# Kernel optimization log

Measured on AMD Instinct MI355X. Metric: run time of the kernel, lower is better.

The kernel has to match this reference:

```python
import jax, jax.numpy as jnp
import numpy as np

B, N, F, E = 2, 50000, 128, 500000


def setup_inputs() -> dict:
    key = jax.random.key(0)
    ks = jax.random.split(key, 7)
    x0 = jax.random.normal(ks[0], (B, N, F), dtype=jnp.float32)
    dst = jax.random.randint(ks[1], (E,), 0, N, dtype=jnp.int32)
    src = jax.random.randint(ks[2], (E,), 0, N, dtype=jnp.int32)
    # torch Linear weights: [out_features, in_features]
    w0 = jax.random.normal(ks[3], (F, 2 * F), dtype=jnp.float32) * 0.05
    b0 = jax.random.normal(ks[4], (F,), dtype=jnp.float32) * 0.05
    w1 = jax.random.normal(ks[5], (F, F), dtype=jnp.float32) * 0.05
    b1 = jax.random.normal(ks[6], (F,), dtype=jnp.float32) * 0.05
    return {"x0": x0, "dst": dst, "src": src, "w0": w0, "b0": b0, "w1": w1, "b1": b1}


def reference(x0, dst, src, w0, b0, w1, b1):
    n = x0.shape[1]
    # gather source node features per edge: [B, E, F] -> [E, B, F] for segment ops
    xe = jnp.transpose(x0[:, src], (1, 0, 2))
    # scatter-reduce over destination nodes (include_self=False semantics)
    s = jax.ops.segment_sum(xe, dst, num_segments=n)                      # [N, B, F]
    mx = jax.ops.segment_max(xe, dst, num_segments=n)                     # [N, B, F]
    cnt = jax.ops.segment_sum(jnp.ones((dst.shape[0],), x0.dtype), dst, num_segments=n)  # [N]
    has_edge = (cnt > 0)[:, None, None]
    x0t = jnp.transpose(x0, (1, 0, 2))                                    # [N, B, F]
    # nodes with no incoming edges keep their original values
    mean = jnp.where(has_edge, s / jnp.maximum(cnt, 1.0)[:, None, None], x0t)
    amax = jnp.where(has_edge, mx, x0t)
    x = jnp.concatenate([mean, amax], axis=-1)                            # [N, B, 2F]
    h = jax.nn.relu(jnp.einsum('nbf,of->nbo', x, w0) + b0)
    # dropout is identity in eval mode
    out = x0t + jnp.einsum('nbf,of->nbo', h, w1) + b1
    return jnp.transpose(out, (1, 0, 2))                                  # [B, N, F]
```

## Files before the change

kernel.cpp:

```cpp
#include <hip/hip_runtime.h>

#define NN 50000
#define FF 128
constexpr int NBF2 = NN * 256;
constexpr int CAP  = 64;

typedef __attribute__((ext_vector_type(4))) short short4v;
typedef __attribute__((ext_vector_type(8))) short short8;
typedef __attribute__((ext_vector_type(4))) float floatx4;

__device__ __forceinline__ unsigned short f2bf(float x) {
    unsigned int u = __float_as_uint(x);
    unsigned int r = (u + 0x7fff + ((u >> 16) & 1)) >> 16;
    return (unsigned short)r;
}
__device__ __forceinline__ float bf2f(short x) {
    return __uint_as_float(((unsigned int)(unsigned short)x) << 16);
}

__global__ __launch_bounds__(256)
void convert_fill(const int* __restrict__ dst, const int* __restrict__ src, int E,
                  const float* __restrict__ x0,
                  const float* __restrict__ w0, const float* __restrict__ w1,
                  int* __restrict__ cursor, int* __restrict__ esrc,
                  unsigned short* __restrict__ x0b,
                  unsigned short* __restrict__ w0b, unsigned short* __restrict__ w1b) {
    int i = blockIdx.x * 256 + threadIdx.x;
    if (i < E) {
        int d = dst[i];
        int pos = atomicAdd(&cursor[d], 1);
        if (pos < CAP) esrc[d * CAP + pos] = src[i];
    }
    int stride = gridDim.x * 256;
    for (int p = i; p < NBF2 / 4; p += stride) {
        int v0 = p * 4;
        int n = v0 >> 8;
        int b = (v0 >> 7) & 1;
        int f = v0 & 127;
        const float4 in = *(const float4*)&x0[(b * NN + n) * FF + f];
        short4v o = { (short)f2bf(in.x), (short)f2bf(in.y), (short)f2bf(in.z), (short)f2bf(in.w) };
        *(short4v*)&x0b[v0] = o;
    }
    if (i < 128 * 256) w0b[i] = f2bf(w0[i]);
    if (i < 128 * 128) w1b[i] = f2bf(w1[i]);
}

constexpr int NPB = 16;
constexpr int XCP = 256 + 8;
constexpr int HSP = 128 + 8;

__global__ __launch_bounds__(256, 4)
void fused_gcn(const unsigned short* __restrict__ x0b,
               const float* __restrict__ x0,
               const int* __restrict__ deg,
               const int* __restrict__ esrc,
               const unsigned short* __restrict__ w0b,
               const float* __restrict__ b0,
               const unsigned short* __restrict__ w1b,
               const float* __restrict__ b1,
               float* __restrict__ out) {
    __shared__ unsigned short xc[32 * XCP];
    __shared__ int sl_hs[32 * HSP / 2];
    __shared__ int cum[17];
    int* sl = sl_hs;
    unsigned short* hs = (unsigned short*)sl_hs;

    int t = threadIdx.x;
    int q = t >> 6;
    int l = t & 63;
    int n0 = blockIdx.x * NPB;

    if (t < 16) cum[t + 1] = min(deg[n0 + t], CAP);
    if (t == 16) cum[0] = 0;
    __syncthreads();
    if (t == 0) {
        int run = 0;
        for (int i = 1; i <= 16; ++i) { run += cum[i]; cum[i] = run; }
    }
    __syncthreads();

    int T = cum[16];
    for (int i = t; i < T + 8; i += 256) {
        if (i < T) {
            int j = 0;
            while (cum[j + 1] <= i) ++j;
            sl[i] = (j << 16) | esrc[(n0 + j) * CAP + (i - cum[j])];
        } else {
            sl[i] = (16 << 16) | 0xFFFF;
        }
    }
    __syncthreads();

    int l4 = l * 4;
    int bb = l >> 5;
    int ff = (l & 31) * 4;
    const float NEG_INF = __int_as_float(0xFF800000);

    int jb = q * 4;
    int nb = n0 + jb;
    int eS = __builtin_amdgcn_readfirstlane(cum[jb]);
    int eE = __builtin_amdgcn_readfirstlane(cum[jb + 4]);

    float sA0=0,sA1=0,sA2=0,sA3=0, sB0=0,sB1=0,sB2=0,sB3=0;
    float sC0=0,sC1=0,sC2=0,sC3=0, sD0=0,sD1=0,sD2=0,sD3=0;
    float mA0=NEG_INF,mA1=NEG_INF,mA2=NEG_INF,mA3=NEG_INF;
    float mB0=NEG_INF,mB1=NEG_INF,mB2=NEG_INF,mB3=NEG_INF;
    float mC0=NEG_INF,mC1=NEG_INF,mC2=NEG_INF,mC3=NEG_INF;
    float mD0=NEG_INF,mD1=NEG_INF,mD2=NEG_INF,mD3=NEG_INF;

#define GATH_K(k) \
    int u##k = __builtin_amdgcn_readfirstlane(sl[e + k]); \
    short4v r##k = *(const short4v*)&x0b[(unsigned)(u##k & 0xffff) * 256 + l4];

#define ACC_K(k) { \
    int ja = u##k >> 16; \
    if ((ja >> 2) == q) { \
        float v0=bf2f(r##k[0]), v1=bf2f(r##k[1]), v2=bf2f(r##k[2]), v3=bf2f(r##k[3]); \
        int g = ja & 3; \
        if (g == 0)      { sA0+=v0;sA1+=v1;sA2+=v2;sA3+=v3; mA0=fmaxf(mA0,v0);mA1=fmaxf(mA1,v1);mA2=fmaxf(mA2,v2);mA3=fmaxf(mA3,v3); } \
        else if (g == 1) { sB0+=v0;sB1+=v1;sB2+=v2;sB3+=v3; mB0=fmaxf(mB0,v0);mB1=fmaxf(mB1,v1);mB2=fmaxf(mB2,v2);mB3=fmaxf(mB3,v3); } \
        else if (g == 2) { sC0+=v0;sC1+=v1;sC2+=v2;sC3+=v3; mC0=fmaxf(mC0,v0);mC1=fmaxf(mC1,v1);mC2=fmaxf(mC2,v2);mC3=fmaxf(mC3,v3); } \
        else             { sD0+=v0;sD1+=v1;sD2+=v2;sD3+=v3; mD0=fmaxf(mD0,v0);mD1=fmaxf(mD1,v1);mD2=fmaxf(mD2,v2);mD3=fmaxf(mD3,v3); } \
    } }

    for (int e = eS; e < eE; e += 8) {
        GATH_K(0) GATH_K(1) GATH_K(2) GATH_K(3)
        GATH_K(4) GATH_K(5) GATH_K(6) GATH_K(7)
        ACC_K(0) ACC_K(1) ACC_K(2) ACC_K(3)
        ACC_K(4) ACC_K(5) ACC_K(6) ACC_K(7)
    }
#undef GATH_K
#undef ACC_K

#define FINAL_G(g, S0,S1,S2,S3, M0,M1,M2,M3) { \
    int dgx = __builtin_amdgcn_readfirstlane(cum[jb + g + 1] - cum[jb + g]); \
    float me0,me1,me2,me3,a0,a1,a2,a3; \
    if (dgx > 0) { \
        float inv = 1.0f / (float)dgx; \
        me0=S0*inv; me1=S1*inv; me2=S2*inv; me3=S3*inv; \
        a0=M0; a1=M1; a2=M2; a3=M3; \
    } else { \
        short4v rr = *(const short4v*)&x0b[(nb + g) * 256 + l4]; \
        me0=a0=bf2f(rr[0]); me1=a1=bf2f(rr[1]); me2=a2=bf2f(rr[2]); me3=a3=bf2f(rr[3]); \
    } \
    int row = (jb + g) * 2 + bb; \
    short4v mv = { (short)f2bf(me0),(short)f2bf(me1),(short)f2bf(me2),(short)f2bf(me3) }; \
    short4v av = { (short)f2bf(a0),(short)f2bf(a1),(short)f2bf(a2),(short)f2bf(a3) }; \
    *(short4v*)&xc[row * XCP + ff]       = mv; \
    *(short4v*)&xc[row * XCP + 128 + ff] = av; \
}
    FINAL_G(0, sA0,sA1,sA2,sA3, mA0,mA1,mA2,mA3)
    FINAL_G(1, sB0,sB1,sB2,sB3, mB0,mB1,mB2,mB3)
    FINAL_G(2, sC0,sC1,sC2,sC3, mC0,mC1,mC2,mC3)
    FINAL_G(3, sD0,sD1,sD2,sD3, mD0,mD1,mD2,mD3)
#undef FINAL_G
    __syncthreads();

    int m    = l & 15;
    int quad = l >> 4;
    int rowbase = (q >> 1) * 16;
    int colbase = (q & 1) * 64;

    floatx4 acc[4];
#pragma unroll
    for (int ct = 0; ct < 4; ++ct) acc[ct] = (floatx4){0.f, 0.f, 0.f, 0.f};
#pragma unroll
    for (int ks = 0; ks < 8; ++ks) {
        short8 a = *(const short8*)&xc[(rowbase + m) * XCP + ks * 32 + quad * 8];
#pragma unroll
        for (int ct = 0; ct < 4; ++ct) {
            short8 bf = *(const short8*)&w0b[(colbase + ct * 16 + m) * 256 + ks * 32 + quad * 8];
            acc[ct] = __builtin_amdgcn_mfma_f32_16x16x32_bf16(a, bf, acc[ct], 0, 0, 0);
        }
    }
#pragma unroll
    for (int ct = 0; ct < 4; ++ct) {
        int col = colbase + ct * 16 + m;
        float bias = b0[col];
#pragma unroll
        for (int r = 0; r < 4; ++r) {
            int row = rowbase + quad * 4 + r;
            hs[row * HSP + col] = f2bf(fmaxf(acc[ct][r] + bias, 0.0f));
        }
    }
    __syncthreads();

    floatx4 acc2[4];
#pragma unroll
    for (int ct = 0; ct < 4; ++ct) acc2[ct] = (floatx4){0.f, 0.f, 0.f, 0.f};
#pragma unroll
    for (int ks = 0; ks < 4; ++ks) {
        short8 a = *(const short8*)&hs[(rowbase + m) * HSP + ks * 32 + quad * 8];
#pragma unroll
        for (int ct = 0; ct < 4; ++ct) {
            short8 bf = *(const short8*)&w1b[(colbase + ct * 16 + m) * 128 + ks * 32 + quad * 8];
            acc2[ct] = __builtin_amdgcn_mfma_f32_16x16x32_bf16(a, bf, acc2[ct], 0, 0, 0);
        }
    }
#pragma unroll
    for (int ct = 0; ct < 4; ++ct) {
        int col = colbase + ct * 16 + m;
        float bias = b1[col];
#pragma unroll
        for (int r = 0; r < 4; ++r) {
            int row = rowbase + quad * 4 + r;
            int n  = n0 + (row >> 1);
            int b2 = row & 1;
            int oi = (b2 * NN + n) * FF + col;
            out[oi] = x0[oi] + bias + acc2[ct][r];
        }
    }
}

extern "C" void kernel_launch(void* const* d_in, const int* in_sizes, int n_in,
                              void* d_out, int out_size, void* d_ws, size_t ws_size,
                              hipStream_t stream) {
    const float* x0  = (const float*)d_in[0];
    const int*   dst = (const int*)d_in[1];
    const int*   src = (const int*)d_in[2];
    const float* w0  = (const float*)d_in[3];
    const float* b0  = (const float*)d_in[4];
    const float* w1  = (const float*)d_in[5];
    const float* b1  = (const float*)d_in[6];
    float* out = (float*)d_out;
    int E = in_sizes[1];

    int* cursor = (int*)d_ws;
    int* esrc   = cursor + NN;
    unsigned short* x0b = (unsigned short*)(esrc + (size_t)NN * CAP);
    unsigned short* w0b = x0b + NBF2;
    unsigned short* w1b = w0b + 128 * 256;

    int eb = (E + 255) / 256;

    hipMemsetAsync(cursor, 0, (size_t)NN * sizeof(int), stream);
    convert_fill<<<eb, 256, 0, stream>>>(dst, src, E, x0, w0, w1, cursor, esrc, x0b, w0b, w1b);
    fused_gcn<<<NN / NPB, 256, 0, stream>>>(x0b, x0, cursor, esrc, w0b, b0, w1b, b1, out);
}
```

Before: 245.7 us.

## Gather fp32 features directly and halve nodes per block

Drops the bf16 copy of x0 that the preprocessing kernel built, so the fused kernel now gathers fp32 rows straight from x0 in its native [B,N,F] layout. This removes a full read-and-write pass over x0, but each gathered element now costs twice the bytes. Nodes per block fall from 16 to 8, which shrinks the MFMA tile to one 16-row tile per block, cuts LDS use and accumulator registers, and raises the occupancy hint to 7. Each block now loads the weight matrices for half as many rows, so weight reloads per node double.

```diff
diff --git a/kernel.cpp b/kernel.cpp
--- a/kernel.cpp
+++ b/kernel.cpp
@@ -2,8 +2,7 @@
 
 #define NN 50000
 #define FF 128
-constexpr int NBF2 = NN * 256;
-constexpr int CAP  = 64;
+constexpr int CAP = 64;
 
 typedef __attribute__((ext_vector_type(4))) short short4v;
 typedef __attribute__((ext_vector_type(8))) short short8;
@@ -14,44 +13,28 @@
     unsigned int r = (u + 0x7fff + ((u >> 16) & 1)) >> 16;
     return (unsigned short)r;
 }
-__device__ __forceinline__ float bf2f(short x) {
-    return __uint_as_float(((unsigned int)(unsigned short)x) << 16);
-}
 
 __global__ __launch_bounds__(256)
-void convert_fill(const int* __restrict__ dst, const int* __restrict__ src, int E,
-                  const float* __restrict__ x0,
-                  const float* __restrict__ w0, const float* __restrict__ w1,
-                  int* __restrict__ cursor, int* __restrict__ esrc,
-                  unsigned short* __restrict__ x0b,
-                  unsigned short* __restrict__ w0b, unsigned short* __restrict__ w1b) {
+void edge_fill(const int* __restrict__ dst, const int* __restrict__ src, int E,
+               const float* __restrict__ w0, const float* __restrict__ w1,
+               int* __restrict__ cursor, int* __restrict__ esrc,
+               unsigned short* __restrict__ w0b, unsigned short* __restrict__ w1b) {
     int i = blockIdx.x * 256 + threadIdx.x;
     if (i < E) {
         int d = dst[i];
         int pos = atomicAdd(&cursor[d], 1);
         if (pos < CAP) esrc[d * CAP + pos] = src[i];
     }
-    int stride = gridDim.x * 256;
-    for (int p = i; p < NBF2 / 4; p += stride) {
-        int v0 = p * 4;
-        int n = v0 >> 8;
-        int b = (v0 >> 7) & 1;
-        int f = v0 & 127;
-        const float4 in = *(const float4*)&x0[(b * NN + n) * FF + f];
-        short4v o = { (short)f2bf(in.x), (short)f2bf(in.y), (short)f2bf(in.z), (short)f2bf(in.w) };
-        *(short4v*)&x0b[v0] = o;
-    }
     if (i < 128 * 256) w0b[i] = f2bf(w0[i]);
     if (i < 128 * 128) w1b[i] = f2bf(w1[i]);
 }
 
-constexpr int NPB = 16;
+constexpr int NPB = 8;
 constexpr int XCP = 256 + 8;
 constexpr int HSP = 128 + 8;
 
-__global__ __launch_bounds__(256, 4)
-void fused_gcn(const unsigned short* __restrict__ x0b,
-               const float* __restrict__ x0,
+__global__ __launch_bounds__(256, 7)
+void fused_gcn(const float* __restrict__ x0,
                const int* __restrict__ deg,
                const int* __restrict__ esrc,
                const unsigned short* __restrict__ w0b,
@@ -59,9 +42,9 @@
                const unsigned short* __restrict__ w1b,
                const float* __restrict__ b1,
                float* __restrict__ out) {
-    __shared__ unsigned short xc[32 * XCP];
-    __shared__ int sl_hs[32 * HSP / 2];
-    __shared__ int cum[17];
+    __shared__ unsigned short xc[16 * XCP];
+    __shared__ int sl_hs[16 * HSP / 2];
+    __shared__ int cum[9];
     int* sl = sl_hs;
     unsigned short* hs = (unsigned short*)sl_hs;
 
@@ -70,57 +53,55 @@
     int l = t & 63;
     int n0 = blockIdx.x * NPB;
 
-    if (t < 16) cum[t + 1] = min(deg[n0 + t], CAP);
-    if (t == 16) cum[0] = 0;
+    if (t < 8) cum[t + 1] = min(deg[n0 + t], CAP);
+    if (t == 8) cum[0] = 0;
     __syncthreads();
     if (t == 0) {
         int run = 0;
-        for (int i = 1; i <= 16; ++i) { run += cum[i]; cum[i] = run; }
-    }
-    __syncthreads();
-
-    int T = cum[16];
+        for (int i = 1; i <= 8; ++i) { run += cum[i]; cum[i] = run; }
+    }
+    __syncthreads();
+
+    int T = cum[8];
     for (int i = t; i < T + 8; i += 256) {
         if (i < T) {
             int j = 0;
             while (cum[j + 1] <= i) ++j;
             sl[i] = (j << 16) | esrc[(n0 + j) * CAP + (i - cum[j])];
         } else {
-            sl[i] = (16 << 16) | 0xFFFF;
-        }
-    }
-    __syncthreads();
-
-    int l4 = l * 4;
+            sl[i] = (NPB << 16);
+        }
+    }
+    __syncthreads();
+
     int bb = l >> 5;
     int ff = (l & 31) * 4;
+    const float* xrow = x0 + (bb * NN) * FF + ff;
     const float NEG_INF = __int_as_float(0xFF800000);
 
-    int jb = q * 4;
+    int jb = q * 2;
     int nb = n0 + jb;
     int eS = __builtin_amdgcn_readfirstlane(cum[jb]);
-    int eE = __builtin_amdgcn_readfirstlane(cum[jb + 4]);
+    int eE = __builtin_amdgcn_readfirstlane(cum[jb + 2]);
 
     float sA0=0,sA1=0,sA2=0,sA3=0, sB0=0,sB1=0,sB2=0,sB3=0;
-    float sC0=0,sC1=0,sC2=0,sC3=0, sD0=0,sD1=0,sD2=0,sD3=0;
     float mA0=NEG_INF,mA1=NEG_INF,mA2=NEG_INF,mA3=NEG_INF;
     float mB0=NEG_INF,mB1=NEG_INF,mB2=NEG_INF,mB3=NEG_INF;
-    float mC0=NEG_INF,mC1=NEG_INF,mC2=NEG_INF,mC3=NEG_INF;
-    float mD0=NEG_INF,mD1=NEG_INF,mD2=NEG_INF,mD3=NEG_INF;
 
 #define GATH_K(k) \
     int u##k = __builtin_amdgcn_readfirstlane(sl[e + k]); \
-    short4v r##k = *(const short4v*)&x0b[(unsigned)(u##k & 0xffff) * 256 + l4];
+    float4 r##k = *(const float4*)&xrow[(u##k & 0xffff) << 7];
 
 #define ACC_K(k) { \
     int ja = u##k >> 16; \
-    if ((ja >> 2) == q) { \
-        float v0=bf2f(r##k[0]), v1=bf2f(r##k[1]), v2=bf2f(r##k[2]), v3=bf2f(r##k[3]); \
-        int g = ja & 3; \
-        if (g == 0)      { sA0+=v0;sA1+=v1;sA2+=v2;sA3+=v3; mA0=fmaxf(mA0,v0);mA1=fmaxf(mA1,v1);mA2=fmaxf(mA2,v2);mA3=fmaxf(mA3,v3); } \
-        else if (g == 1) { sB0+=v0;sB1+=v1;sB2+=v2;sB3+=v3; mB0=fmaxf(mB0,v0);mB1=fmaxf(mB1,v1);mB2=fmaxf(mB2,v2);mB3=fmaxf(mB3,v3); } \
-        else if (g == 2) { sC0+=v0;sC1+=v1;sC2+=v2;sC3+=v3; mC0=fmaxf(mC0,v0);mC1=fmaxf(mC1,v1);mC2=fmaxf(mC2,v2);mC3=fmaxf(mC3,v3); } \
-        else             { sD0+=v0;sD1+=v1;sD2+=v2;sD3+=v3; mD0=fmaxf(mD0,v0);mD1=fmaxf(mD1,v1);mD2=fmaxf(mD2,v2);mD3=fmaxf(mD3,v3); } \
+    if ((ja >> 1) == q) { \
+        if ((ja & 1) == 0) { \
+            sA0+=r##k.x; sA1+=r##k.y; sA2+=r##k.z; sA3+=r##k.w; \
+            mA0=fmaxf(mA0,r##k.x); mA1=fmaxf(mA1,r##k.y); mA2=fmaxf(mA2,r##k.z); mA3=fmaxf(mA3,r##k.w); \
+        } else { \
+            sB0+=r##k.x; sB1+=r##k.y; sB2+=r##k.z; sB3+=r##k.w; \
+            mB0=fmaxf(mB0,r##k.x); mB1=fmaxf(mB1,r##k.y); mB2=fmaxf(mB2,r##k.z); mB3=fmaxf(mB3,r##k.w); \
+        } \
     } }
 
     for (int e = eS; e < eE; e += 8) {
@@ -140,8 +121,8 @@
         me0=S0*inv; me1=S1*inv; me2=S2*inv; me3=S3*inv; \
         a0=M0; a1=M1; a2=M2; a3=M3; \
     } else { \
-        short4v rr = *(const short4v*)&x0b[(nb + g) * 256 + l4]; \
-        me0=a0=bf2f(rr[0]); me1=a1=bf2f(rr[1]); me2=a2=bf2f(rr[2]); me3=a3=bf2f(rr[3]); \
+        float4 rr = *(const float4*)&xrow[(nb + g) << 7]; \
+        me0=a0=rr.x; me1=a1=rr.y; me2=a2=rr.z; me3=a3=rr.w; \
     } \
     int row = (jb + g) * 2 + bb; \
     short4v mv = { (short)f2bf(me0),(short)f2bf(me1),(short)f2bf(me2),(short)f2bf(me3) }; \
@@ -151,59 +132,56 @@
 }
     FINAL_G(0, sA0,sA1,sA2,sA3, mA0,mA1,mA2,mA3)
     FINAL_G(1, sB0,sB1,sB2,sB3, mB0,mB1,mB2,mB3)
-    FINAL_G(2, sC0,sC1,sC2,sC3, mC0,mC1,mC2,mC3)
-    FINAL_G(3, sD0,sD1,sD2,sD3, mD0,mD1,mD2,mD3)
 #undef FINAL_G
     __syncthreads();
 
     int m    = l & 15;
     int quad = l >> 4;
-    int rowbase = (q >> 1) * 16;
-    int colbase = (q & 1) * 64;
-
-    floatx4 acc[4];
-#pragma unroll
-    for (int ct = 0; ct < 4; ++ct) acc[ct] = (floatx4){0.f, 0.f, 0.f, 0.f};
+    int colbase = q * 32;
+
+    floatx4 acc[2];
+#pragma unroll
+    for (int ct = 0; ct < 2; ++ct) acc[ct] = (floatx4){0.f, 0.f, 0.f, 0.f};
 #pragma unroll
     for (int ks = 0; ks < 8; ++ks) {
-        short8 a = *(const short8*)&xc[(rowbase + m) * XCP + ks * 32 + quad * 8];
-#pragma unroll
-        for (int ct = 0; ct < 4; ++ct) {
-            short8 bf = *(const short8*)&w0b[(colbase + ct * 16 + m) * 256 + ks * 32 + quad * 8];
-            acc[ct] = __builtin_amdgcn_mfma_f32_16x16x32_bf16(a, bf, acc[ct], 0, 0, 0);
-        }
-    }
-#pragma unroll
-    for (int ct = 0; ct < 4; ++ct) {
+        short8 a = *(const short8*)&xc[m * XCP + ks * 32 + quad * 8];
+#pragma unroll
+        for (int ct = 0; ct < 2; ++ct) {
+            short8 bfr = *(const short8*)&w0b[(colbase + ct * 16 + m) * 256 + ks * 32 + quad * 8];
+            acc[ct] = __builtin_amdgcn_mfma_f32_16x16x32_bf16(a, bfr, acc[ct], 0, 0, 0);
+        }
+    }
+#pragma unroll
+    for (int ct = 0; ct < 2; ++ct) {
         int col = colbase + ct * 16 + m;
         float bias = b0[col];
 #pragma unroll
         for (int r = 0; r < 4; ++r) {
-            int row = rowbase + quad * 4 + r;
+            int row = quad * 4 + r;
             hs[row * HSP + col] = f2bf(fmaxf(acc[ct][r] + bias, 0.0f));
         }
     }
     __syncthreads();
 
-    floatx4 acc2[4];
-#pragma unroll
-    for (int ct = 0; ct < 4; ++ct) acc2[ct] = (floatx4){0.f, 0.f, 0.f, 0.f};
+    floatx4 acc2[2];
+#pragma unroll
+    for (int ct = 0; ct < 2; ++ct) acc2[ct] = (floatx4){0.f, 0.f, 0.f, 0.f};
 #pragma unroll
     for (int ks = 0; ks < 4; ++ks) {
-        short8 a = *(const short8*)&hs[(rowbase + m) * HSP + ks * 32 + quad * 8];
-#pragma unroll
-        for (int ct = 0; ct < 4; ++ct) {
-            short8 bf = *(const short8*)&w1b[(colbase + ct * 16 + m) * 128 + ks * 32 + quad * 8];
-            acc2[ct] = __builtin_amdgcn_mfma_f32_16x16x32_bf16(a, bf, acc2[ct], 0, 0, 0);
-        }
-    }
-#pragma unroll
-    for (int ct = 0; ct < 4; ++ct) {
+        short8 a = *(const short8*)&hs[m * HSP + ks * 32 + quad * 8];
+#pragma unroll
+        for (int ct = 0; ct < 2; ++ct) {
+            short8 bfr = *(const short8*)&w1b[(colbase + ct * 16 + m) * 128 + ks * 32 + quad * 8];
+            acc2[ct] = __builtin_amdgcn_mfma_f32_16x16x32_bf16(a, bfr, acc2[ct], 0, 0, 0);
+        }
+    }
+#pragma unroll
+    for (int ct = 0; ct < 2; ++ct) {
         int col = colbase + ct * 16 + m;
         float bias = b1[col];
 #pragma unroll
         for (int r = 0; r < 4; ++r) {
-            int row = rowbase + quad * 4 + r;
+            int row = quad * 4 + r;
             int n  = n0 + (row >> 1);
             int b2 = row & 1;
             int oi = (b2 * NN + n) * FF + col;
@@ -227,13 +205,12 @@
 
     int* cursor = (int*)d_ws;
     int* esrc   = cursor + NN;
-    unsigned short* x0b = (unsigned short*)(esrc + (size_t)NN * CAP);
-    unsigned short* w0b = x0b + NBF2;
+    unsigned short* w0b = (unsigned short*)(esrc + (size_t)NN * CAP);
     unsigned short* w1b = w0b + 128 * 256;
 
     int eb = (E + 255) / 256;
 
     hipMemsetAsync(cursor, 0, (size_t)NN * sizeof(int), stream);
-    convert_fill<<<eb, 256, 0, stream>>>(dst, src, E, x0, w0, w1, cursor, esrc, x0b, w0b, w1b);
-    fused_gcn<<<NN / NPB, 256, 0, stream>>>(x0b, x0, cursor, esrc, w0b, b0, w1b, b1, out);
-}
+    edge_fill<<<eb, 256, 0, stream>>>(dst, src, E, w0, w1, cursor, esrc, w0b, w1b);
+    fused_gcn<<<NN / NPB, 256, 0, stream>>>(x0, cursor, esrc, w0b, b0, w1b, b1, out);
+}
```

Result: faster. 232.3 us (-5.5%).
